# Performance work log

Measured on AMD Instinct MI355X. Metric: run time of the kernel, lower is better.

## Reference

```python
import jax, jax.numpy as jnp
import numpy as np

N, D = 65536, 256


def _unit(x):
    # contrastive embeddings are L2-normalized; also keeps exp(dot) finite
    return x / jnp.linalg.norm(x, axis=-1, keepdims=True)


def setup_inputs() -> dict:
    key = jax.random.key(0)
    k1, k2 = jax.random.split(key)
    z_a = _unit(jax.random.normal(k1, (N, D), dtype=jnp.float32))
    z_b = _unit(jax.random.normal(k2, (N, D), dtype=jnp.float32))
    return {"z_a": z_a, "z_b": z_b}


def reference(z_a, z_b):
    # d_i = dot(z_a[i], z_b[i])  (the only quantity the original ever computes)
    n = z_a.shape[0]
    d = jnp.sum(z_a * z_b, axis=-1)  # [n]
    # Original loop structure:
    #   alignment      = sum_i (-d_i)
    #   negative_sum_i = (# of j in range(n-1), j != i) * d_i
    #                  = (n-2) * d_i for i < n-1, (n-1) * d_i for i == n-1
    #   uniformity_i   = exp(d_i)
    counts = jnp.full((n,), n - 2, dtype=d.dtype).at[n - 1].set(n - 1)
    return jnp.sum((counts - 1.0) * d + jnp.exp(d))
```

## Files before the change

### kernel.cpp

```cpp
#include <hip/hip_runtime.h>
#include <math.h>


#define D_DIM 256
#define ROWS 4
#define BLOCKS 4096

__global__ __launch_bounds__(256)
void dot_loss(const float* __restrict__ za,
              const float* __restrict__ zb,
              float* __restrict__ out,
              int n) {
    const int lane = threadIdx.x & 63;
    const int wave = threadIdx.x >> 6;
    const int waveId = blockIdx.x * 4 + wave;
    const int row0 = waveId * ROWS;

    const float4* a4 = (const float4*)za + (size_t)row0 * 64 + lane;
    const float4* b4 = (const float4*)zb + (size_t)row0 * 64 + lane;

    float4 av[ROWS], bv[ROWS];
    #pragma unroll
    for (int r = 0; r < ROWS; ++r) av[r] = a4[(size_t)r * 64];
    #pragma unroll
    for (int r = 0; r < ROWS; ++r) bv[r] = b4[(size_t)r * 64];

    float d[ROWS];
    #pragma unroll
    for (int r = 0; r < ROWS; ++r) {
        float t = av[r].x * bv[r].x;
        t = fmaf(av[r].y, bv[r].y, t);
        t = fmaf(av[r].z, bv[r].z, t);
        t = fmaf(av[r].w, bv[r].w, t);
        d[r] = t;
    }

    #pragma unroll
    for (int off = 32; off > 0; off >>= 1) {
        #pragma unroll
        for (int r = 0; r < ROWS; ++r)
            d[r] += __shfl_down(d[r], off);
    }

    float acc = 0.0f;
    if (lane == 0) {
        #pragma unroll
        for (int r = 0; r < ROWS; ++r) {
            int row = row0 + r;
            float coeff = (row == n - 1) ? (float)(n - 2) : (float)(n - 3);
            acc += coeff * d[r] + expf(d[r]);
        }
    }

    __shared__ float smem[4];
    if (lane == 0) smem[wave] = acc;
    __syncthreads();
    if (threadIdx.x == 0)
        atomicAdd(out, smem[0] + smem[1] + smem[2] + smem[3]);
}

extern "C" void kernel_launch(void* const* d_in, const int* in_sizes, int n_in,
                              void* d_out, int out_size, void* d_ws, size_t ws_size,
                              hipStream_t stream) {
    const float* za = (const float*)d_in[0];
    const float* zb = (const float*)d_in[1];
    float* out = (float*)d_out;
    const int n = in_sizes[0] / D_DIM;

    hipMemsetAsync(out, 0, sizeof(float), stream);
    dot_loss<<<BLOCKS, 256, 0, stream>>>(za, zb, out, n);
}
```

Baseline: 165.2 us.

## Replace atomic accumulation with per-block partials and a separate reduction kernel

Each wave now handles 8 rows instead of 4 and the grid is halved. Loads of a and b are interleaved, and an occupancy hint is added to launch bounds. Blocks write partial sums to workspace instead of doing a global atomicAdd, and a second single-block kernel sums them in double precision, which also drops the memset. The aim is to remove atomic contention and deepen memory-level parallelism, at the cost of an extra kernel launch and more registers per thread.

```diff
diff --git a/kernel.cpp b/kernel.cpp
--- a/kernel.cpp
+++ b/kernel.cpp
@@ -3,27 +3,28 @@
 
 
 #define D_DIM 256
-#define ROWS 4
-#define BLOCKS 4096
+#define ROWS 8
+#define BLOCKS 2048
 
-__global__ __launch_bounds__(256)
-void dot_loss(const float* __restrict__ za,
-              const float* __restrict__ zb,
-              float* __restrict__ out,
-              int n) {
+__global__ __launch_bounds__(256, 4)
+void dot_loss_partial(const float4* __restrict__ za4,
+                      const float4* __restrict__ zb4,
+                      float* __restrict__ partial,
+                      int n) {
     const int lane = threadIdx.x & 63;
     const int wave = threadIdx.x >> 6;
     const int waveId = blockIdx.x * 4 + wave;
     const int row0 = waveId * ROWS;
 
-    const float4* a4 = (const float4*)za + (size_t)row0 * 64 + lane;
-    const float4* b4 = (const float4*)zb + (size_t)row0 * 64 + lane;
+    const float4* a = za4 + (size_t)row0 * 64 + lane;
+    const float4* b = zb4 + (size_t)row0 * 64 + lane;
 
     float4 av[ROWS], bv[ROWS];
     #pragma unroll
-    for (int r = 0; r < ROWS; ++r) av[r] = a4[(size_t)r * 64];
-    #pragma unroll
-    for (int r = 0; r < ROWS; ++r) bv[r] = b4[(size_t)r * 64];
+    for (int r = 0; r < ROWS; ++r) {
+        av[r] = a[(size_t)r * 64];
+        bv[r] = b[(size_t)r * 64];
+    }
 
     float d[ROWS];
     #pragma unroll
@@ -56,17 +57,37 @@
     if (lane == 0) smem[wave] = acc;
     __syncthreads();
     if (threadIdx.x == 0)
-        atomicAdd(out, smem[0] + smem[1] + smem[2] + smem[3]);
+        partial[blockIdx.x] = smem[0] + smem[1] + smem[2] + smem[3];
+}
+
+__global__ __launch_bounds__(256)
+void reduce_partials(const float* __restrict__ partial,
+                     float* __restrict__ out,
+                     int m) {
+    const int lane = threadIdx.x & 63;
+    const int wave = threadIdx.x >> 6;
+    double s = 0.0;
+    for (int i = threadIdx.x; i < m; i += 256)
+        s += (double)partial[i];
+    #pragma unroll
+    for (int off = 32; off > 0; off >>= 1)
+        s += __shfl_down(s, off);
+    __shared__ double smem[4];
+    if (lane == 0) smem[wave] = s;
+    __syncthreads();
+    if (threadIdx.x == 0)
+        out[0] = (float)(smem[0] + smem[1] + smem[2] + smem[3]);
 }
 
 extern "C" void kernel_launch(void* const* d_in, const int* in_sizes, int n_in,
                               void* d_out, int out_size, void* d_ws, size_t ws_size,
                               hipStream_t stream) {
-    const float* za = (const float*)d_in[0];
-    const float* zb = (const float*)d_in[1];
+    const float4* za4 = (const float4*)d_in[0];
+    const float4* zb4 = (const float4*)d_in[1];
     float* out = (float*)d_out;
+    float* partial = (float*)d_ws;
     const int n = in_sizes[0] / D_DIM;
 
-    hipMemsetAsync(out, 0, sizeof(float), stream);
-    dot_loss<<<BLOCKS, 256, 0, stream>>>(za, zb, out, n);
+    dot_loss_partial<<<BLOCKS, 256, 0, stream>>>(za4, zb4, partial, n);
+    reduce_partials<<<1, 256, 0, stream>>>(partial, out, BLOCKS);
 }
```

Measured after the change: 147.4 us. -10.8%, faster.
